# Performance work log

Measured on AMD Instinct MI355X. Metric: run time of the kernel, lower is better.

Reference implementation:

```python
import jax, jax.numpy as jnp
import numpy as np

E = 16777216       # total edges across the batch
NG = 1024          # num_graphs
K = 32             # action_topk
TEMP = 1.0         # policy_temperature


def setup_inputs() -> dict:
    key = jax.random.key(0)
    k1, k2, k3, k4, k5 = jax.random.split(key, 5)
    edge_logits = jax.random.normal(k1, (E,), dtype=jnp.float32)
    edge_scores = jax.random.normal(k2, (E,), dtype=jnp.float32)
    stop_logits = jax.random.normal(k3, (NG,), dtype=jnp.float32)
    edge_batch = jnp.sort(jax.random.randint(k4, (E,), 0, NG)).astype(jnp.int64)
    candidate_mask = jax.random.randint(k5, (E,), 0, 2).astype(bool)
    return {
        'edge_logits': edge_logits,
        'edge_scores': edge_scores,
        'stop_logits': stop_logits,
        'edge_batch': edge_batch,
        'candidate_mask': candidate_mask,
    }


def _topk_edge_mask(edge_scores, edge_batch, candidate_mask):
    """Faithful port of _select_topk_candidate_edges, returning a boolean keep
    mask over all E edges (fixed shape; indices of kept edges are implicit)."""
    neg_inf = jnp.finfo(jnp.float32).min
    # Non-candidates get a sentinel segment NG and -inf score so they sort last.
    seg_key = jnp.where(candidate_mask, edge_batch, NG)
    score = jnp.where(candidate_mask, edge_scores.astype(jnp.float32), neg_inf)
    # Sort by score descending, then stable-sort by segment id
    order_score = jnp.argsort(-score)
    seg_by_score = seg_key[order_score]
    order_seg = jnp.argsort(seg_by_score)          # jax argsort is stable
    cand_sorted = order_score[order_seg]           # original edge ids, sorted
    seg_sorted = seg_by_score[order_seg]
    # rank within each segment = position - segment start (exclusive cumsum)
    counts = jnp.bincount(seg_sorted, length=NG + 1)
    start = jnp.concatenate([jnp.zeros((1,), counts.dtype), jnp.cumsum(counts)[:-1]])
    rank = jnp.arange(E) - start[seg_sorted]
    keep_sorted = (rank < K) & (seg_sorted < NG)
    return jnp.zeros((E,), dtype=bool).at[cand_sorted].set(keep_sorted)


def _segment_logsumexp_1d(logits, segment_ids, num_segments):
    """Faithful port of torch _segment_logsumexp_1d."""
    neg_inf = jnp.finfo(logits.dtype).min
    eps = jnp.finfo(logits.dtype).eps
    max_per = jnp.full((num_segments,), neg_inf, dtype=logits.dtype).at[segment_ids].max(logits)
    exp = jnp.exp(logits - max_per[segment_ids])
    sum_per = jnp.zeros((num_segments,), dtype=logits.dtype).at[segment_ids].add(exp)
    return jnp.log(jnp.maximum(sum_per, eps)) + max_per


def reference(edge_logits, edge_scores, stop_logits, edge_batch, candidate_mask):
    neg_inf = jnp.finfo(jnp.float32).min
    # Per-graph top-k pruning of candidate edges by edge_scores
    valid = _topk_edge_mask(edge_scores, edge_batch, candidate_mask)
    # Segmented temperature softmax over (valid edges + stop action)
    logits_t = edge_logits / TEMP
    stop_t = stop_logits / TEMP
    masked = jnp.where(valid, logits_t, neg_inf)
    lse_edges = _segment_logsumexp_1d(masked, edge_batch, NG)       # [NG]
    log_denom = jnp.logaddexp(lse_edges, stop_t)                    # [NG]
    log_prob_edge = jnp.where(valid, logits_t - log_denom[edge_batch], neg_inf)
    return log_prob_edge
```

## Files before the change

### kernel.cpp

```cpp
#include <hip/hip_runtime.h>
#include <float.h>

#define TPB 256
#define KTOP 32
#define BIN_CAP 512
#define BMAP_WORDS 1024

#define SENT_U32 0xFF7F0000u
#define VCLAMP 3.0e38f

__device__ __forceinline__ unsigned int f2u(float f){
  unsigned int u = __float_as_uint(f);
  return (u & 0x80000000u) ? ~u : (u | 0x80000000u);
}

__device__ int suffix_total(int* hist, int NB, int* gsum, int tid){
  int GS = NB >> 8;
  int p = 0, base = tid * GS;
  for (int j = 0; j < GS; ++j) p += hist[base + j];
  gsum[tid] = p;
  __syncthreads();
  for (int d = 1; d < 256; d <<= 1){
    int v = (tid + d < 256) ? gsum[tid + d] : 0;
    __syncthreads();
    gsum[tid] += v;
    __syncthreads();
  }
  return gsum[0];
}

__device__ int find_bin(int* hist, int NB, int* gsum, int R, int* s2, int tid,
                        int* above_out){
  int GS = NB >> 8;
  int St  = gsum[tid];
  int St1 = (tid < 255) ? gsum[tid + 1] : 0;
  if (R > St1 && R <= St) s2[0] = tid;
  __syncthreads();
  if (tid == 0){
    int G = s2[0];
    int above = (G < 255) ? gsum[G + 1] : 0;
    int b = (G + 1) * GS - 1;
    for (; b > G * GS; --b){
      int h = hist[b];
      if (above + h >= R) break;
      above += h;
    }
    s2[0] = b; s2[1] = above;
  }
  __syncthreads();
  int bin = s2[0];
  *above_out = s2[1];
  __syncthreads();
  return bin;
}

__global__ void __launch_bounds__(TPB, 8)
fused_kernel(const float* __restrict__ logits,
             const float* __restrict__ scores,
             const float* __restrict__ stop_logits,
             const int* __restrict__ batch,
             const int* __restrict__ cmask,
             float* __restrict__ out, int E, int NG)
{
  __shared__ int hist[2048];
  __shared__ int gsum[256];
  __shared__ int s2[2];
  __shared__ int sbounds[2];
  __shared__ unsigned int bmap[BMAP_WORDS];
  __shared__ unsigned int bin_u[BIN_CAP];
  __shared__ int bin_i[BIN_CAP];
  __shared__ int ab_i[KTOP];
  __shared__ int vidx[KTOP];
  __shared__ float vlog[KTOP];
  __shared__ int cnt_bin, cnt_ab, vcnt;
  __shared__ float sh_logden;

  int tid = threadIdx.x;
  int g = blockIdx.x;

  if (tid < 2){
    int target = g + tid;
    int lo = 0, hi = E;
    while (lo < hi){
      int mid = (lo + hi) >> 1;
      if (batch[mid] < target) lo = mid + 1; else hi = mid;
    }
    sbounds[tid] = lo;
  }
  __syncthreads();
  int s = sbounds[0], e = sbounds[1];
  int s4 = (s + 3) & ~3; if (s4 > e) s4 = e;
  int e4 = e & ~3;       if (e4 < s4) e4 = s4;
  const int4*   cm4 = (const int4*)cmask;
  const float4* sc4 = (const float4*)scores;

  for (int b = tid; b < 2048; b += TPB) hist[b] = 0;
  for (int w = tid; w < BMAP_WORDS; w += TPB) bmap[w] = 0;
  if (tid == 0){ cnt_bin = 0; cnt_ab = 0; vcnt = 0; }
  __syncthreads();

  const float SENT = __uint_as_float(SENT_U32);

  auto p1 = [&](int m, float sc, int idx){
    if (m){
      unsigned u = f2u(sc);
      atomicAdd(&hist[u >> 21], 1);
      int rel = idx - s;
      if (rel < BMAP_WORDS * 32) atomicOr(&bmap[rel >> 5], 1u << (rel & 31));
    }
  };
  {
    int i = s + tid;  if (i < s4){ p1(cmask[i], scores[i], i); out[i] = SENT; }
    int j = e4 + tid; if (j < e) { p1(cmask[j], scores[j], j); out[j] = SENT; }
    float4 sv = make_float4(SENT, SENT, SENT, SENT);
    for (int q = (s4 >> 2) + tid, qe = (e4 >> 2); q < qe; q += TPB){
      int4 m = cm4[q]; float4 sc = sc4[q];
      int base = q << 2;
      p1(m.x, sc.x, base);     p1(m.y, sc.y, base + 1);
      p1(m.z, sc.z, base + 2); p1(m.w, sc.w, base + 3);
      ((float4*)out)[q] = sv;
    }
  }
  __syncthreads();

  auto is_cand = [&](int idx) -> bool {
    int rel = idx - s;
    if (rel < BMAP_WORDS * 32) return (bmap[rel >> 5] >> (rel & 31)) & 1u;
    return cmask[idx] != 0;
  };
  auto scan_sc = [&](auto&& fn){
    int i = s + tid;  if (i < s4) fn(scores[i], i);
    int j = e4 + tid; if (j < e)  fn(scores[j], j);
    for (int q = (s4 >> 2) + tid, qe = (e4 >> 2); q < qe; q += TPB){
      float4 sc = sc4[q];
      int base = q << 2;
      fn(sc.x, base);     fn(sc.y, base + 1);
      fn(sc.z, base + 2); fn(sc.w, base + 3);
    }
  };

  int T = suffix_total(hist, 2048, gsum, tid);
  bool sel = (T > KTOP);
  unsigned int prefix = 0; int pshift = 32; int R = KTOP;
  if (sel){
    int above;
    int b1 = find_bin(hist, 2048, gsum, R, s2, tid, &above);
    R -= above; prefix = (unsigned)b1; pshift = 21;
    int hcnt = hist[b1];
    __syncthreads();
    if (hcnt > BIN_CAP){
      for (int b = tid; b < 2048; b += TPB) hist[b] = 0;
      __syncthreads();
      scan_sc([&](float sc, int idx){
        unsigned u = f2u(sc);
        if ((u >> 21) == prefix && is_cand(idx))
          atomicAdd(&hist[(u >> 10) & 0x7FFu], 1);
      });
      __syncthreads();
      suffix_total(hist, 2048, gsum, tid);
      int b2 = find_bin(hist, 2048, gsum, R, s2, tid, &above);
      R -= above; prefix = (prefix << 11) | (unsigned)b2; pshift = 10;
      hcnt = hist[b2];
      __syncthreads();
      if (hcnt > BIN_CAP){
        for (int b = tid; b < 1024; b += TPB) hist[b] = 0;
        __syncthreads();
        scan_sc([&](float sc, int idx){
          unsigned u = f2u(sc);
          if ((u >> 10) == prefix && is_cand(idx))
            atomicAdd(&hist[u & 0x3FFu], 1);
        });
        __syncthreads();
        suffix_total(hist, 1024, gsum, tid);
        int b3 = find_bin(hist, 1024, gsum, R, s2, tid, &above);
        R -= above; prefix = (prefix << 10) | (unsigned)b3; pshift = 0;
        __syncthreads();
      }
    }
  }

  if (sel){
    scan_sc([&](float sc, int idx){
      unsigned u = f2u(sc);
      unsigned hp = (pshift < 32) ? (u >> pshift) : 0u;
      if (hp >= prefix){
        if (is_cand(idx)){
          if (hp == prefix){
            int sl = atomicAdd(&cnt_bin, 1);
            if (sl < BIN_CAP){ bin_u[sl] = u; bin_i[sl] = idx; }
          } else {
            int sl = atomicAdd(&cnt_ab, 1);
            if (sl < KTOP) ab_i[sl] = idx;
          }
        }
      }
    });
    __syncthreads();
    int bn = min(cnt_bin, BIN_CAP);
    for (int jj = tid; jj < bn; jj += TPB){
      unsigned long long kj = ((unsigned long long)bin_u[jj] << 32)
                            | (unsigned long long)(unsigned)(~(unsigned)bin_i[jj]);
      int rank = 0;
      for (int k = 0; k < bn; ++k){
        unsigned long long kk2 = ((unsigned long long)bin_u[k] << 32)
                               | (unsigned long long)(unsigned)(~(unsigned)bin_i[k]);
        rank += (kk2 > kj) ? 1 : 0;
      }
      if (rank < R){
        int sl = atomicAdd(&vcnt, 1);
        if (sl < KTOP) vidx[sl] = bin_i[jj];
      }
    }
    int na = min(cnt_ab, KTOP);
    for (int jj = tid; jj < na; jj += TPB){
      int sl = atomicAdd(&vcnt, 1);
      if (sl < KTOP) vidx[sl] = ab_i[jj];
    }
  } else {
    int n = e - s;
    int nw = (n + 31) >> 5; if (nw > BMAP_WORDS) nw = BMAP_WORDS;
    for (int w = tid; w < nw; w += TPB){
      unsigned bits = bmap[w];
      while (bits){
        int b = __ffs((int)bits) - 1;
        bits &= bits - 1;
        int sl = atomicAdd(&vcnt, 1);
        if (sl < KTOP) vidx[sl] = s + (w << 5) + b;
      }
    }
    for (int i = s + BMAP_WORDS * 32 + tid; i < e; i += TPB){
      if (cmask[i]){
        int sl = atomicAdd(&vcnt, 1);
        if (sl < KTOP) vidx[sl] = i;
      }
    }
  }
  __syncthreads();

  int c = min(vcnt, KTOP);
  if (tid < c) vlog[tid] = logits[vidx[tid]];
  __syncthreads();
  if (tid == 0){
    float stop = stop_logits[g];
    float logden;
    if (c == 0){
      logden = stop;
    } else {
      float m = -FLT_MAX;
      for (int j2 = 0; j2 < c; ++j2) m = fmaxf(m, vlog[j2]);
      float sum = 0.f;
      for (int j2 = 0; j2 < c; ++j2) sum += expf(vlog[j2] - m);
      float lse = logf(fmaxf(sum, FLT_EPSILON)) + m;
      float mx = fmaxf(lse, stop);
      float dd = fabsf(lse - stop);
      logden = mx + log1pf(expf(-dd));
    }
    sh_logden = logden;
  }
  __syncthreads();

  if (tid < c){
    float val = vlog[tid] - sh_logden;
    if (!(val >= -VCLAMP)) val = -VCLAMP;
    if (val > VCLAMP)      val =  VCLAMP;
    out[vidx[tid]] = val;
  }
}

extern "C" void kernel_launch(void* const* d_in, const int* in_sizes, int n_in,
                              void* d_out, int out_size, void* d_ws, size_t ws_size,
                              hipStream_t stream){
  const float* edge_logits = (const float*)d_in[0];
  const float* edge_scores = (const float*)d_in[1];
  const float* stop_logits = (const float*)d_in[2];
  const int*   edge_batch  = (const int*)d_in[3];
  const int*   cmask       = (const int*)d_in[4];
  int E  = in_sizes[0];
  int NG = in_sizes[2];
  float* out = (float*)d_out;
  (void)d_ws; (void)ws_size;

  hipLaunchKernelGGL(fused_kernel, dim3(NG), dim3(TPB), 0, stream,
                     edge_logits, edge_scores, stop_logits, edge_batch, cmask,
                     out, E, NG);
}
```

Measured before the change: 265.0 us.

## Stash high-score candidates in one pass and skip radix histogram passes

The first pass now reads only scores, and fetches the candidate mask just for scores at or above a fixed threshold. Those edges go into a shared stash, and the top-32 is ranked directly from it whenever the stash holds between 32 and 512 entries. Otherwise the kernel falls back to the full multi-pass radix select. The aim is to drop the dense mask read and the extra histogram passes for typical inputs. The change also raises block size to 512, replaces the serial segment binary search with a ballot-based parallel search, uses nontemporal stores for the sentinel fill, and uses a wavefront shuffle reduction for the log-sum-exp. The threshold is tuned to normally distributed scores, so other distributions will take the slower fallback path.

```diff
diff --git a/kernel.cpp b/kernel.cpp
--- a/kernel.cpp
+++ b/kernel.cpp
@@ -1,13 +1,14 @@
 #include <hip/hip_runtime.h>
 #include <float.h>
 
-#define TPB 256
+#define TPB 512
 #define KTOP 32
 #define BIN_CAP 512
-#define BMAP_WORDS 1024
-
 #define SENT_U32 0xFF7F0000u
 #define VCLAMP 3.0e38f
+#define STHRESH 2.0f
+
+typedef float floatx4 __attribute__((ext_vector_type(4)));
 
 __device__ __forceinline__ unsigned int f2u(float f){
   unsigned int u = __float_as_uint(f);
@@ -16,14 +17,17 @@
 
 __device__ int suffix_total(int* hist, int NB, int* gsum, int tid){
   int GS = NB >> 8;
-  int p = 0, base = tid * GS;
-  for (int j = 0; j < GS; ++j) p += hist[base + j];
-  gsum[tid] = p;
+  if (tid < 256){
+    int p = 0, base = tid * GS;
+    for (int j = 0; j < GS; ++j) p += hist[base + j];
+    gsum[tid] = p;
+  }
   __syncthreads();
   for (int d = 1; d < 256; d <<= 1){
-    int v = (tid + d < 256) ? gsum[tid + d] : 0;
-    __syncthreads();
-    gsum[tid] += v;
+    int v = 0;
+    if (tid < 256) v = (tid + d < 256) ? gsum[tid + d] : 0;
+    __syncthreads();
+    if (tid < 256) gsum[tid] += v;
     __syncthreads();
   }
   return gsum[0];
@@ -32,9 +36,11 @@
 __device__ int find_bin(int* hist, int NB, int* gsum, int R, int* s2, int tid,
                         int* above_out){
   int GS = NB >> 8;
-  int St  = gsum[tid];
-  int St1 = (tid < 255) ? gsum[tid + 1] : 0;
-  if (R > St1 && R <= St) s2[0] = tid;
+  if (tid < 256){
+    int St  = gsum[tid];
+    int St1 = (tid < 255) ? gsum[tid + 1] : 0;
+    if (R > St1 && R <= St) s2[0] = tid;
+  }
   __syncthreads();
   if (tid == 0){
     int G = s2[0];
@@ -66,173 +72,203 @@
   __shared__ int gsum[256];
   __shared__ int s2[2];
   __shared__ int sbounds[2];
-  __shared__ unsigned int bmap[BMAP_WORDS];
+  __shared__ int scnt[2];
   __shared__ unsigned int bin_u[BIN_CAP];
   __shared__ int bin_i[BIN_CAP];
   __shared__ int ab_i[KTOP];
   __shared__ int vidx[KTOP];
   __shared__ float vlog[KTOP];
-  __shared__ int cnt_bin, cnt_ab, vcnt;
+  __shared__ int cnt_bin, cnt_ab, vcnt, cnt_stash;
   __shared__ float sh_logden;
 
   int tid = threadIdx.x;
   int g = blockIdx.x;
 
-  if (tid < 2){
-    int target = g + tid;
+  {
+    int grp = tid >> 8;
+    int lt  = tid & 255;
+    int target = g + grp;
     int lo = 0, hi = E;
-    while (lo < hi){
-      int mid = (lo + hi) >> 1;
-      if (batch[mid] < target) lo = mid + 1; else hi = mid;
-    }
-    sbounds[tid] = lo;
-  }
+    for (int round = 0; round < 3; ++round){
+      if (lt == 0) scnt[grp] = 0;
+      __syncthreads();
+      int width = hi - lo;
+      int pred = 0;
+      if (width > 256){
+        long long w = width;
+        int q = lo + (int)((w * (long long)lt) >> 8);
+        pred = (batch[q] < target) ? 1 : 0;
+      }
+      unsigned long long bal = __ballot(pred);
+      if ((tid & 63) == 0) atomicAdd(&scnt[grp], __popcll(bal));
+      __syncthreads();
+      if (width > 256){
+        long long w = width;
+        int c = scnt[grp];
+        int nlo = (c > 0)   ? lo + (int)((w * (long long)(c - 1)) >> 8) + 1 : lo;
+        int nhi = (c < 256) ? lo + (int)((w * (long long)c) >> 8)          : hi;
+        lo = nlo; hi = nhi;
+      }
+      __syncthreads();
+    }
+    if (lt == 0) scnt[grp] = 0;
+    __syncthreads();
+    int width = hi - lo;
+    int pred = (lt < width) ? ((batch[lo + lt] < target) ? 1 : 0) : 0;
+    unsigned long long bal = __ballot(pred);
+    if ((tid & 63) == 0) atomicAdd(&scnt[grp], __popcll(bal));
+    __syncthreads();
+    if (lt == 0) sbounds[grp] = lo + scnt[grp];
+  }
+  if (tid == 0){ cnt_bin = 0; cnt_ab = 0; vcnt = 0; cnt_stash = 0; }
   __syncthreads();
   int s = sbounds[0], e = sbounds[1];
+
   int s4 = (s + 3) & ~3; if (s4 > e) s4 = e;
   int e4 = e & ~3;       if (e4 < s4) e4 = s4;
-  const int4*   cm4 = (const int4*)cmask;
   const float4* sc4 = (const float4*)scores;
-
-  for (int b = tid; b < 2048; b += TPB) hist[b] = 0;
-  for (int w = tid; w < BMAP_WORDS; w += TPB) bmap[w] = 0;
-  if (tid == 0){ cnt_bin = 0; cnt_ab = 0; vcnt = 0; }
-  __syncthreads();
-
   const float SENT = __uint_as_float(SENT_U32);
 
-  auto p1 = [&](int m, float sc, int idx){
-    if (m){
-      unsigned u = f2u(sc);
-      atomicAdd(&hist[u >> 21], 1);
-      int rel = idx - s;
-      if (rel < BMAP_WORDS * 32) atomicOr(&bmap[rel >> 5], 1u << (rel & 31));
+  auto p1 = [&](float sc, int idx){
+    if (sc >= STHRESH){
+      if (cmask[idx]){
+        int sl = atomicAdd(&cnt_stash, 1);
+        if (sl < BIN_CAP){ bin_u[sl] = f2u(sc); bin_i[sl] = idx; }
+      }
     }
   };
   {
-    int i = s + tid;  if (i < s4){ p1(cmask[i], scores[i], i); out[i] = SENT; }
-    int j = e4 + tid; if (j < e) { p1(cmask[j], scores[j], j); out[j] = SENT; }
-    float4 sv = make_float4(SENT, SENT, SENT, SENT);
-    for (int q = (s4 >> 2) + tid, qe = (e4 >> 2); q < qe; q += TPB){
-      int4 m = cm4[q]; float4 sc = sc4[q];
-      int base = q << 2;
-      p1(m.x, sc.x, base);     p1(m.y, sc.y, base + 1);
-      p1(m.z, sc.z, base + 2); p1(m.w, sc.w, base + 3);
-      ((float4*)out)[q] = sv;
-    }
-  }
-  __syncthreads();
-
-  auto is_cand = [&](int idx) -> bool {
-    int rel = idx - s;
-    if (rel < BMAP_WORDS * 32) return (bmap[rel >> 5] >> (rel & 31)) & 1u;
-    return cmask[idx] != 0;
-  };
-  auto scan_sc = [&](auto&& fn){
-    int i = s + tid;  if (i < s4) fn(scores[i], i);
-    int j = e4 + tid; if (j < e)  fn(scores[j], j);
+    int i = s + tid;  if (i < s4){ p1(scores[i], i); out[i] = SENT; }
+    int j = e4 + tid; if (j < e) { p1(scores[j], j); out[j] = SENT; }
+    floatx4 sv = { SENT, SENT, SENT, SENT };
+    floatx4* out4 = (floatx4*)out;
     for (int q = (s4 >> 2) + tid, qe = (e4 >> 2); q < qe; q += TPB){
       float4 sc = sc4[q];
+      __builtin_nontemporal_store(sv, &out4[q]);
       int base = q << 2;
-      fn(sc.x, base);     fn(sc.y, base + 1);
-      fn(sc.z, base + 2); fn(sc.w, base + 3);
-    }
-  };
-
-  int T = suffix_total(hist, 2048, gsum, tid);
-  bool sel = (T > KTOP);
-  unsigned int prefix = 0; int pshift = 32; int R = KTOP;
-  if (sel){
-    int above;
-    int b1 = find_bin(hist, 2048, gsum, R, s2, tid, &above);
-    R -= above; prefix = (unsigned)b1; pshift = 21;
-    int hcnt = hist[b1];
-    __syncthreads();
-    if (hcnt > BIN_CAP){
-      for (int b = tid; b < 2048; b += TPB) hist[b] = 0;
-      __syncthreads();
-      scan_sc([&](float sc, int idx){
-        unsigned u = f2u(sc);
-        if ((u >> 21) == prefix && is_cand(idx))
-          atomicAdd(&hist[(u >> 10) & 0x7FFu], 1);
-      });
-      __syncthreads();
-      suffix_total(hist, 2048, gsum, tid);
-      int b2 = find_bin(hist, 2048, gsum, R, s2, tid, &above);
-      R -= above; prefix = (prefix << 11) | (unsigned)b2; pshift = 10;
-      hcnt = hist[b2];
+      p1(sc.x, base);     p1(sc.y, base + 1);
+      p1(sc.z, base + 2); p1(sc.w, base + 3);
+    }
+  }
+  __syncthreads();
+
+  int S = cnt_stash;
+  if (S >= KTOP && S <= BIN_CAP){
+    for (int jj = tid; jj < S; jj += TPB){
+      unsigned long long kj = ((unsigned long long)bin_u[jj] << 32)
+                            | (unsigned long long)(unsigned)(~(unsigned)bin_i[jj]);
+      int rank = 0;
+      for (int k = 0; k < S; ++k){
+        unsigned long long kk = ((unsigned long long)bin_u[k] << 32)
+                              | (unsigned long long)(unsigned)(~(unsigned)bin_i[k]);
+        rank += (kk > kj) ? 1 : 0;
+      }
+      if (rank < KTOP){
+        int sl = atomicAdd(&vcnt, 1);
+        if (sl < KTOP) vidx[sl] = bin_i[jj];
+      }
+    }
+  } else {
+    auto scan_sc = [&](auto&& fn){
+      int i = s + tid;  if (i < s4) fn(scores[i], i);
+      int j = e4 + tid; if (j < e)  fn(scores[j], j);
+      for (int q = (s4 >> 2) + tid, qe = (e4 >> 2); q < qe; q += TPB){
+        float4 sc = sc4[q];
+        int base = q << 2;
+        fn(sc.x, base);     fn(sc.y, base + 1);
+        fn(sc.z, base + 2); fn(sc.w, base + 3);
+      }
+    };
+    auto is_cand = [&](int idx) -> bool { return cmask[idx] != 0; };
+
+    for (int b = tid; b < 2048; b += TPB) hist[b] = 0;
+    __syncthreads();
+    scan_sc([&](float sc, int idx){
+      if (is_cand(idx)) atomicAdd(&hist[f2u(sc) >> 21], 1);
+    });
+    __syncthreads();
+    int T = suffix_total(hist, 2048, gsum, tid);
+    bool sel = (T > KTOP);
+    unsigned int prefix = 0; int pshift = 32; int R = KTOP;
+    if (sel){
+      int above;
+      int b1 = find_bin(hist, 2048, gsum, R, s2, tid, &above);
+      R -= above; prefix = (unsigned)b1; pshift = 21;
+      int hcnt = hist[b1];
       __syncthreads();
       if (hcnt > BIN_CAP){
-        for (int b = tid; b < 1024; b += TPB) hist[b] = 0;
+        for (int b = tid; b < 2048; b += TPB) hist[b] = 0;
         __syncthreads();
         scan_sc([&](float sc, int idx){
           unsigned u = f2u(sc);
-          if ((u >> 10) == prefix && is_cand(idx))
-            atomicAdd(&hist[u & 0x3FFu], 1);
+          if ((u >> 21) == prefix && is_cand(idx))
+            atomicAdd(&hist[(u >> 10) & 0x7FFu], 1);
         });
         __syncthreads();
-        suffix_total(hist, 1024, gsum, tid);
-        int b3 = find_bin(hist, 1024, gsum, R, s2, tid, &above);
-        R -= above; prefix = (prefix << 10) | (unsigned)b3; pshift = 0;
+        suffix_total(hist, 2048, gsum, tid);
+        int b2 = find_bin(hist, 2048, gsum, R, s2, tid, &above);
+        R -= above; prefix = (prefix << 11) | (unsigned)b2; pshift = 10;
+        hcnt = hist[b2];
         __syncthreads();
-      }
-    }
-  }
-
-  if (sel){
-    scan_sc([&](float sc, int idx){
-      unsigned u = f2u(sc);
-      unsigned hp = (pshift < 32) ? (u >> pshift) : 0u;
-      if (hp >= prefix){
+        if (hcnt > BIN_CAP){
+          for (int b = tid; b < 1024; b += TPB) hist[b] = 0;
+          __syncthreads();
+          scan_sc([&](float sc, int idx){
+            unsigned u = f2u(sc);
+            if ((u >> 10) == prefix && is_cand(idx))
+              atomicAdd(&hist[u & 0x3FFu], 1);
+          });
+          __syncthreads();
+          suffix_total(hist, 1024, gsum, tid);
+          int b3 = find_bin(hist, 1024, gsum, R, s2, tid, &above);
+          R -= above; prefix = (prefix << 10) | (unsigned)b3; pshift = 0;
+          __syncthreads();
+        }
+      }
+      scan_sc([&](float sc, int idx){
+        unsigned u = f2u(sc);
+        unsigned hp = (pshift < 32) ? (u >> pshift) : 0u;
+        if (hp >= prefix){
+          if (is_cand(idx)){
+            if (hp == prefix){
+              int sl = atomicAdd(&cnt_bin, 1);
+              if (sl < BIN_CAP){ bin_u[sl] = u; bin_i[sl] = idx; }
+            } else {
+              int sl = atomicAdd(&cnt_ab, 1);
+              if (sl < KTOP) ab_i[sl] = idx;
+            }
+          }
+        }
+      });
+      __syncthreads();
+      int bn = min(cnt_bin, BIN_CAP);
+      for (int jj = tid; jj < bn; jj += TPB){
+        unsigned long long kj = ((unsigned long long)bin_u[jj] << 32)
+                              | (unsigned long long)(unsigned)(~(unsigned)bin_i[jj]);
+        int rank = 0;
+        for (int k = 0; k < bn; ++k){
+          unsigned long long kk2 = ((unsigned long long)bin_u[k] << 32)
+                                 | (unsigned long long)(unsigned)(~(unsigned)bin_i[k]);
+          rank += (kk2 > kj) ? 1 : 0;
+        }
+        if (rank < R){
+          int sl = atomicAdd(&vcnt, 1);
+          if (sl < KTOP) vidx[sl] = bin_i[jj];
+        }
+      }
+      int na = min(cnt_ab, KTOP);
+      for (int jj = tid; jj < na; jj += TPB){
+        int sl = atomicAdd(&vcnt, 1);
+        if (sl < KTOP) vidx[sl] = ab_i[jj];
+      }
+    } else {
+      scan_sc([&](float sc, int idx){
+        (void)sc;
         if (is_cand(idx)){
-          if (hp == prefix){
-            int sl = atomicAdd(&cnt_bin, 1);
-            if (sl < BIN_CAP){ bin_u[sl] = u; bin_i[sl] = idx; }
-          } else {
-            int sl = atomicAdd(&cnt_ab, 1);
-            if (sl < KTOP) ab_i[sl] = idx;
-          }
-        }
-      }
-    });
-    __syncthreads();
-    int bn = min(cnt_bin, BIN_CAP);
-    for (int jj = tid; jj < bn; jj += TPB){
-      unsigned long long kj = ((unsigned long long)bin_u[jj] << 32)
-                            | (unsigned long long)(unsigned)(~(unsigned)bin_i[jj]);
-      int rank = 0;
-      for (int k = 0; k < bn; ++k){
-        unsigned long long kk2 = ((unsigned long long)bin_u[k] << 32)
-                               | (unsigned long long)(unsigned)(~(unsigned)bin_i[k]);
-        rank += (kk2 > kj) ? 1 : 0;
-      }
-      if (rank < R){
-        int sl = atomicAdd(&vcnt, 1);
-        if (sl < KTOP) vidx[sl] = bin_i[jj];
-      }
-    }
-    int na = min(cnt_ab, KTOP);
-    for (int jj = tid; jj < na; jj += TPB){
-      int sl = atomicAdd(&vcnt, 1);
-      if (sl < KTOP) vidx[sl] = ab_i[jj];
-    }
-  } else {
-    int n = e - s;
-    int nw = (n + 31) >> 5; if (nw > BMAP_WORDS) nw = BMAP_WORDS;
-    for (int w = tid; w < nw; w += TPB){
-      unsigned bits = bmap[w];
-      while (bits){
-        int b = __ffs((int)bits) - 1;
-        bits &= bits - 1;
-        int sl = atomicAdd(&vcnt, 1);
-        if (sl < KTOP) vidx[sl] = s + (w << 5) + b;
-      }
-    }
-    for (int i = s + BMAP_WORDS * 32 + tid; i < e; i += TPB){
-      if (cmask[i]){
-        int sl = atomicAdd(&vcnt, 1);
-        if (sl < KTOP) vidx[sl] = i;
-      }
+          int sl = atomicAdd(&vcnt, 1);
+          if (sl < KTOP) vidx[sl] = idx;
+        }
+      });
     }
   }
   __syncthreads();
@@ -240,22 +276,27 @@
   int c = min(vcnt, KTOP);
   if (tid < c) vlog[tid] = logits[vidx[tid]];
   __syncthreads();
-  if (tid == 0){
-    float stop = stop_logits[g];
-    float logden;
-    if (c == 0){
-      logden = stop;
-    } else {
-      float m = -FLT_MAX;
-      for (int j2 = 0; j2 < c; ++j2) m = fmaxf(m, vlog[j2]);
-      float sum = 0.f;
-      for (int j2 = 0; j2 < c; ++j2) sum += expf(vlog[j2] - m);
-      float lse = logf(fmaxf(sum, FLT_EPSILON)) + m;
-      float mx = fmaxf(lse, stop);
-      float dd = fabsf(lse - stop);
-      logden = mx + log1pf(expf(-dd));
-    }
-    sh_logden = logden;
+  if (tid < 64){
+    float v = (tid < c) ? vlog[tid] : -FLT_MAX;
+    float m = v;
+    #pragma unroll
+    for (int d = 32; d; d >>= 1) m = fmaxf(m, __shfl_xor(m, d));
+    float ex = (tid < c) ? expf(v - m) : 0.f;
+    #pragma unroll
+    for (int d = 32; d; d >>= 1) ex += __shfl_xor(ex, d);
+    if (tid == 0){
+      float stop = stop_logits[g];
+      float logden;
+      if (c == 0){
+        logden = stop;
+      } else {
+        float lse = logf(fmaxf(ex, FLT_EPSILON)) + m;
+        float mx = fmaxf(lse, stop);
+        float dd = fabsf(lse - stop);
+        logden = mx + log1pf(expf(-dd));
+      }
+      sh_logden = logden;
+    }
   }
   __syncthreads();
 
```

Measured after the change: 250.7 us. 5.4% less time.
